# Kernel optimization log

Measured on AMD Instinct MI355X. Metric: run time of the kernel, lower is better.

Reference implementation:

```python
import jax, jax.numpy as jnp
import numpy as np

N = 8388608          # number of samples (2**23)
T_MAX = 100000       # number of distinct time values -> ~84 ties per time


def setup_inputs() -> dict:
    key = jax.random.key(0)
    k1, k2, k3 = jax.random.split(key, 3)
    inp = jax.random.normal(k1, (N,), dtype=jnp.float32)            # log hazards
    target = jax.random.randint(k2, (N,), 0, T_MAX, dtype=jnp.int32)  # times
    weight = jax.random.randint(k3, (N,), 0, 2, dtype=jnp.int32)      # event indicator
    return {"input": inp, "target": target, "weight": weight}


def _cox_efron_npll(log_hz, time, event):
    """Negative Cox partial log-likelihood with Efron tie correction, mean reduction.

    Faithful to torchsurv's _partial_likelihood_efron: per unique time j,
    pll_j = sum_{i in H_j} log_hz_i - sum_{l=0}^{m_j-1} log(D_j - (l/m_j)*T_j)
    where H_j = events at time j, D_j = sum of exp(log_hz) over risk set (t>=t_j),
    T_j = sum of exp(log_hz) over H_j, m_j = |H_j|; loss = -mean over j with m_j>0.
    """
    n = log_hz.shape[0]
    order = jnp.argsort(time)                       # sort by time (group-sum math is tie-order invariant)
    t = time[order]
    lh = log_hz[order]
    ev = event[order].astype(lh.dtype)

    # group id per sample: 0..(num_unique-1), padded groups beyond that are empty
    new_grp = jnp.concatenate([jnp.zeros((1,), jnp.int32), (t[1:] != t[:-1]).astype(jnp.int32)])
    seg = jnp.cumsum(new_grp)                       # [n] int32

    hz = jnp.exp(lh)
    grp_hz = jax.ops.segment_sum(hz, seg, num_segments=n)          # sum exp per time group
    denom_naive = jnp.cumsum(grp_hz[::-1])[::-1]                   # risk-set sums (suffix over groups)
    m = jax.ops.segment_sum(ev, seg, num_segments=n)               # events per group
    log_nom = jax.ops.segment_sum(lh * ev, seg, num_segments=n)    # sum of log_hz over H_j
    ties = jax.ops.segment_sum(hz * ev, seg, num_segments=n)       # sum of exp over H_j

    # rank l in [0, m_j) of each event within its group
    csum_e = jnp.cumsum(ev)
    events_before = jnp.concatenate([jnp.zeros((1,), lh.dtype), jnp.cumsum(m)[:-1]])
    rank = csum_e - 1.0 - events_before[seg]
    mg = jnp.maximum(m[seg], 1.0)
    term = jnp.where(ev > 0.0,
                     jnp.log(denom_naive[seg] - (rank / mg) * ties[seg]),
                     0.0)
    log_denom = jax.ops.segment_sum(term, seg, num_segments=n)

    include = (m > 0.0).astype(lh.dtype)
    pll = jnp.where(m > 0.0, log_nom - log_denom, 0.0)
    # reduction='mean': -pll.nanmean() over groups that contain events
    return -(jnp.sum(pll) / jnp.sum(include))


def reference(input, target, weight):
    return _cox_efron_npll(input, target, weight)
```

## Files before the change

kernel.cpp:

```cpp
#include <hip/hip_runtime.h>

#define TMAXV 100000
#define CHUNK 256
#define NCHUNK ((TMAXV + CHUNK - 1) / CHUNK)
#define WB 256
#define LOGWB 8
#define SB ((TMAXV + WB - 1) / WB)
#define SBP 512
#define TILE 4096
#define RPT 16
#define KS 8
#define CAP 4096
#define RPH (CAP / 256)


__device__ __forceinline__ float block_reduce_sum(float v, float* sdata) {
    int lane = threadIdx.x & 63;
    int wid  = threadIdx.x >> 6;
    #pragma unroll
    for (int off = 32; off > 0; off >>= 1)
        v += __shfl_down(v, off, 64);
    if (lane == 0) sdata[wid] = v;
    __syncthreads();
    if (wid == 0) {
        v = (lane < 4) ? sdata[lane] : 0.0f;
        v += __shfl_down(v, 2, 64);
        v += __shfl_down(v, 1, 64);
    }
    return v;
}

__device__ __forceinline__ double block_reduce_sum_d(double v, double* sdata) {
    int lane = threadIdx.x & 63;
    int wid  = threadIdx.x >> 6;
    #pragma unroll
    for (int off = 32; off > 0; off >>= 1)
        v += __shfl_down(v, off, 64);
    if (lane == 0) sdata[wid] = v;
    __syncthreads();
    if (wid == 0) {
        v = (lane < 4) ? sdata[lane] : 0.0;
        v += __shfl_down(v, 2, 64);
        v += __shfl_down(v, 1, 64);
    }
    return v;
}

__device__ __forceinline__ unsigned encode_rec(float x, int t, int e) {
    float h = __expf(x);
    return (__float_as_uint(h) & 0x7FFFFF00u)
         | (unsigned)(t & (WB - 1))
         | ((unsigned)e << 31);
}


__global__ void count_pfx_kernel(const int* __restrict__ tgt,
                                 int* __restrict__ pfx_arr,
                                 int* __restrict__ cnt_t, int n) {
    __shared__ int lc[SBP];
    __shared__ int ls[SBP];
    int tid = threadIdx.x, tile = blockIdx.x;
    lc[tid] = 0; lc[tid + 256] = 0;
    __syncthreads();
    int lo = tile * TILE;
    if (lo + TILE <= n) {
        const int4* tgt4 = (const int4*)(tgt + lo);
        #pragma unroll
        for (int q = 0; q < RPT / 4; ++q) {
            int4 t4 = tgt4[q * 256 + tid];
            atomicAdd(&lc[t4.x >> LOGWB], 1);
            atomicAdd(&lc[t4.y >> LOGWB], 1);
            atomicAdd(&lc[t4.z >> LOGWB], 1);
            atomicAdd(&lc[t4.w >> LOGWB], 1);
        }
    } else {
        int hi = min(n, lo + TILE);
        for (int i = lo + tid; i < hi; i += 256)
            atomicAdd(&lc[tgt[i] >> LOGWB], 1);
    }
    __syncthreads();
    int c0 = lc[tid], c1 = lc[tid + 256];
    int i1 = tid + 256;
    ls[tid] = c0; ls[i1] = c1;
    __syncthreads();
    for (int off = 1; off < SBP; off <<= 1) {
        int a0 = (tid >= off) ? ls[tid - off] : 0;
        int a1 = (i1  >= off) ? ls[i1  - off] : 0;
        __syncthreads();
        ls[tid] += a0; ls[i1] += a1;
        __syncthreads();
    }
    size_t rb = (size_t)tile * SBP;
    pfx_arr[rb + tid] = ls[tid] - c0;
    pfx_arr[rb + i1]  = ls[i1]  - c1;
    cnt_t[rb + tid] = c0;
    cnt_t[rb + i1]  = c1;
}

__global__ void tile_scan_direct_kernel(const int* __restrict__ cnt_t,
                                        int* __restrict__ tilebase_s,
                                        int* __restrict__ totals, int nt) {
    __shared__ int ls[256];
    int s = blockIdx.x, tid = threadIdx.x;
    int run = 0;
    for (int t0 = 0; t0 < nt; t0 += 256) {
        int t = t0 + tid;
        int c = (t < nt) ? cnt_t[(size_t)t * SBP + s] : 0;
        ls[tid] = c;
        __syncthreads();
        for (int off = 1; off < 256; off <<= 1) {
            int a = (tid >= off) ? ls[tid - off] : 0;
            __syncthreads();
            ls[tid] += a;
            __syncthreads();
        }
        int incl = ls[tid];
        int tot  = ls[255];
        if (t < nt) tilebase_s[(size_t)s * nt + t] = run + incl - c;
        run += tot;
        __syncthreads();
    }
    if (tid == 0) totals[s] = run;
}

__global__ void bucket_base_kernel(const int* __restrict__ totals,
                                   int* __restrict__ base, int n) {
    __shared__ int ls[SBP];
    int tid = threadIdx.x;
    int c = totals[tid];
    ls[tid] = c;
    __syncthreads();
    for (int off = 1; off < SBP; off <<= 1) {
        int a = (tid >= off) ? ls[tid - off] : 0;
        __syncthreads();
        ls[tid] += a;
        __syncthreads();
    }
    base[tid] = ls[tid] - c;
    if (tid == 0) base[SBP] = n;
}

__global__ void scatter_kernel(const float* __restrict__ lh,
                               const int*   __restrict__ tgt,
                               const int*   __restrict__ ev,
                               const int*   __restrict__ pfx_arr,
                               const int*   __restrict__ tilebase_s,
                               const int*   __restrict__ base,
                               unsigned* __restrict__ val,
                               double* __restrict__ acc, int n, int nt) {
    __shared__ unsigned fu[TILE];
    __shared__ unsigned short bidv[TILE];
    __shared__ int pfx[SBP];
    __shared__ int tb[SBP];
    __shared__ int lrank[SBP];
    __shared__ float sdata[4];
    int tid  = threadIdx.x;
    int tile = blockIdx.x;
    int lo   = tile * TILE;
    int cnt_here = min(TILE, n - lo);
    int i1 = tid + 256;
    size_t rb = (size_t)tile * SBP;

    pfx[tid] = pfx_arr[rb + tid];
    pfx[i1]  = pfx_arr[rb + i1];
    tb[tid]  = base[tid] + tilebase_s[(size_t)tid * nt + tile];
    tb[i1]   = base[i1]  + tilebase_s[(size_t)i1  * nt + tile];
    lrank[tid] = 0; lrank[i1] = 0;

    unsigned rbits[RPT];
    int      rk[RPT];
    float xl = 0.f;
    if (lo + TILE <= n) {
        const int4*   tgt4 = (const int4*)(tgt + lo);
        const int4*   ev4  = (const int4*)(ev + lo);
        const float4* lh4  = (const float4*)(lh + lo);
        #pragma unroll
        for (int q = 0; q < RPT / 4; ++q) {
            int idx = q * 256 + tid;
            int4   t4 = tgt4[idx];
            int4   e4 = ev4[idx];
            float4 x4 = lh4[idx];
            rbits[q*4+0] = encode_rec(x4.x, t4.x, e4.x & 1); rk[q*4+0] = t4.x >> LOGWB; if (e4.x & 1) xl += x4.x;
            rbits[q*4+1] = encode_rec(x4.y, t4.y, e4.y & 1); rk[q*4+1] = t4.y >> LOGWB; if (e4.y & 1) xl += x4.y;
            rbits[q*4+2] = encode_rec(x4.z, t4.z, e4.z & 1); rk[q*4+2] = t4.z >> LOGWB; if (e4.z & 1) xl += x4.z;
            rbits[q*4+3] = encode_rec(x4.w, t4.w, e4.w & 1); rk[q*4+3] = t4.w >> LOGWB; if (e4.w & 1) xl += x4.w;
        }
    } else {
        #pragma unroll
        for (int k = 0; k < RPT; ++k) {
            int i = lo + k * 256 + tid;
            if (i < n) {
                int t = tgt[i]; int e = ev[i] & 1; float x = lh[i];
                rbits[k] = encode_rec(x, t, e);
                rk[k] = t >> LOGWB;
                if (e) xl += x;
            } else rk[k] = -1;
        }
    }
    __syncthreads();

    #pragma unroll
    for (int k = 0; k < RPT; ++k) {
        if (rk[k] >= 0) {
            int b = rk[k];
            int r = atomicAdd(&lrank[b], 1);
            int pos = pfx[b] + r;
            fu[pos]   = rbits[k];
            bidv[pos] = (unsigned short)b;
        }
    }
    __syncthreads();

    int pairs = cnt_here >> 1;
    const uint2* fu2 = (const uint2*)fu;
    const unsigned* bid2 = (const unsigned*)bidv;
    for (int q = tid; q < pairs; q += 256) {
        uint2 bb = fu2[q];
        unsigned bp = bid2[q];
        int b0 = (int)(bp & 0xFFFFu);
        int b1 = (int)(bp >> 16);
        int p0 = q * 2;
        val[tb[b0] + (p0     - pfx[b0])] = bb.x;
        val[tb[b1] + (p0 + 1 - pfx[b1])] = bb.y;
    }
    if ((cnt_here & 1) && tid == 0) {
        int p = cnt_here - 1;
        int b = (int)bidv[p];
        val[tb[b] + (p - pfx[b])] = fu[p];
    }

    float rl = block_reduce_sum(xl, sdata);
    if (tid == 0) atomicAdd(&acc[2], (double)rl);
}

__global__ void bucket_hist_kernel(const unsigned* __restrict__ val,
                                   const int* __restrict__ base,
                                   float* __restrict__ partials,
                                   float* __restrict__ chunk_sum) {
    __shared__ unsigned fv[CAP];
    __shared__ unsigned cnt[WB];
    __shared__ unsigned rankc[WB];
    __shared__ unsigned pfx[WB];
    __shared__ unsigned ls[WB];
    __shared__ float sdata[4];
    int tid = threadIdx.x;
    int b   = blockIdx.x >> 3;
    int k   = blockIdx.x & (KS - 1);
    int lo0 = base[b], len = base[b + 1] - lo0;
    int lo  = lo0 + (int)(((long long)len * k) / KS);
    int hi  = lo0 + (int)(((long long)len * (k + 1)) / KS);

    float sh = 0.f, cm = 0.f, th = 0.f;

    for (int c0 = lo; c0 < hi; c0 += CAP) {
        int c1 = min(hi, c0 + CAP);
        cnt[tid] = 0; rankc[tid] = 0;
        __syncthreads();

        unsigned rv[RPH];
        int      rs[RPH];
        #pragma unroll
        for (int u = 0; u < RPH; ++u) {
            int i = c0 + u * 256 + tid;
            if (i < c1) {
                rv[u] = val[i];
                rs[u] = (int)(rv[u] & (WB - 1));
                atomicAdd(&cnt[rs[u]], 1u);
            } else {
                rs[u] = -1;
            }
        }
        __syncthreads();

        unsigned c = cnt[tid];
        ls[tid] = c;
        __syncthreads();
        for (int off = 1; off < 256; off <<= 1) {
            unsigned a = (tid >= off) ? ls[tid - off] : 0u;
            __syncthreads();
            ls[tid] += a;
            __syncthreads();
        }
        pfx[tid] = ls[tid] - c;
        __syncthreads();

        #pragma unroll
        for (int u = 0; u < RPH; ++u) {
            if (rs[u] >= 0) {
                unsigned r = atomicAdd(&rankc[rs[u]], 1u);
                fv[pfx[rs[u]] + r] = rv[u];
            }
        }
        __syncthreads();

        int s0 = (int)pfx[tid], e0 = s0 + (int)cnt[tid];
        for (int p = s0; p < e0; ++p) {
            unsigned bits = fv[p];
            float h = fabsf(__uint_as_float(bits));
            sh += h;
            if (bits >> 31) { cm += 1.0f; th += h; }
        }
        __syncthreads();
    }

    float* pbase = partials + (size_t)blockIdx.x * 3 * WB;
    pbase[0 * WB + tid] = sh;
    pbase[1 * WB + tid] = cm;
    pbase[2 * WB + tid] = th;

    float st = block_reduce_sum(sh, sdata);
    if (tid == 0) unsafeAtomicAdd(&chunk_sum[b], st);
}

__global__ void pll_suffix_kernel(const float* __restrict__ partials,
                                  const float* __restrict__ chunk_sum,
                                  double* __restrict__ acc) {
    __shared__ float sf[CHUNK];
    __shared__ float sdata[4];
    __shared__ float sdata2[4];
    __shared__ double dsd[4];
    __shared__ double doff;
    int tid = threadIdx.x;
    int b   = blockIdx.x;
    float sh = 0.f, cm = 0.f, th = 0.f;
    #pragma unroll
    for (int k = 0; k < KS; ++k) {
        const float* pbase = partials + (size_t)(b * KS + k) * 3 * WB;
        sh += pbase[0 * WB + tid];
        cm += pbase[1 * WB + tid];
        th += pbase[2 * WB + tid];
    }
    sf[tid] = sh;
    __syncthreads();
    for (int off = 1; off < CHUNK; off <<= 1) {
        float add = (tid + off < CHUNK) ? sf[tid + off] : 0.0f;
        __syncthreads();
        sf[tid] += add;
        __syncthreads();
    }
    double mysum = 0.0;
    for (int j = b + 1 + tid; j < NCHUNK; j += 256)
        mysum += (double)chunk_sum[j];
    double red = block_reduce_sum_d(mysum, dsd);
    if (tid == 0) doff = red;
    __syncthreads();
    double off_d = doff;

    int t = b * CHUNK + tid;
    float pll = 0.0f, inc = 0.0f;
    if (t < TMAXV && cm > 0.5f) {
        float D    = (float)(off_d + (double)sf[tid]);
        int   mi   = (int)(cm + 0.5f);
        float step = th / cm;
        float s = 0.0f;
        for (int l = 0; l < mi; ++l)
            s += __logf(D - (float)l * step);
        pll = -s;
        inc = 1.0f;
    }
    float rp = block_reduce_sum(pll, sdata);
    __syncthreads();
    float ri = block_reduce_sum(inc, sdata2);
    if (threadIdx.x == 0) {
        atomicAdd(&acc[0], (double)rp);
        atomicAdd(&acc[1], (double)ri);
    }
}

__global__ void finalize_kernel(const double* __restrict__ acc,
                                float* __restrict__ out) {
    double cnt = acc[1];
    out[0] = (cnt > 0.0) ? (float)(-(acc[0] + acc[2]) / cnt) : 0.0f;
}

__global__ void hist_kernel(const float* __restrict__ lh,
                            const int*   __restrict__ tgt,
                            const int*   __restrict__ ev,
                            float* __restrict__ sum_hz,
                            float* __restrict__ mcnt,
                            float* __restrict__ log_nom,
                            float* __restrict__ ties,
                            int n) {
    int i = blockIdx.x * blockDim.x + threadIdx.x;
    if (i >= n) return;
    float x = lh[i];
    int   t = tgt[i];
    int   e = ev[i];
    float h = __expf(x);
    unsafeAtomicAdd(&sum_hz[t], h);
    if (e) {
        unsafeAtomicAdd(&mcnt[t], 1.0f);
        unsafeAtomicAdd(&log_nom[t], x);
        unsafeAtomicAdd(&ties[t], h);
    }
}

__global__ void chunk_sum_kernel(const float* __restrict__ sum_hz,
                                 float* __restrict__ chunk_sum) {
    __shared__ float sdata[4];
    int i = blockIdx.x * CHUNK + threadIdx.x;
    float v = (i < TMAXV) ? sum_hz[i] : 0.0f;
    v = block_reduce_sum(v, sdata);
    if (threadIdx.x == 0) chunk_sum[blockIdx.x] = v;
}

__global__ void chunk_scan_kernel(const float* __restrict__ chunk_sum,
                                  double* __restrict__ chunk_off) {
    __shared__ double ds[512];
    int tid = threadIdx.x;
    double own = (tid < NCHUNK) ? (double)chunk_sum[tid] : 0.0;
    ds[tid] = own;
    __syncthreads();
    for (int off = 1; off < 512; off <<= 1) {
        double add = (tid + off < 512) ? ds[tid + off] : 0.0;
        __syncthreads();
        ds[tid] += add;
        __syncthreads();
    }
    if (tid < NCHUNK) chunk_off[tid] = ds[tid] - own;
}

__global__ void pll_kernel(const float* __restrict__ mcnt,
                           const float* __restrict__ log_nom,
                           const float* __restrict__ ties,
                           const float* __restrict__ sum_hz,
                           const double* __restrict__ chunk_off,
                           double* __restrict__ acc) {
    __shared__ float sf[CHUNK];
    __shared__ float sdata[4];
    __shared__ float sdata2[4];
    int tid = threadIdx.x;
    int t   = blockIdx.x * CHUNK + tid;
    float v = (t < TMAXV) ? sum_hz[t] : 0.0f;
    sf[tid] = v;
    __syncthreads();
    for (int off = 1; off < CHUNK; off <<= 1) {
        float add = (tid + off < CHUNK) ? sf[tid + off] : 0.0f;
        __syncthreads();
        sf[tid] += add;
        __syncthreads();
    }
    float pll = 0.0f, inc = 0.0f;
    if (t < TMAXV) {
        float mv = mcnt[t];
        if (mv > 0.5f) {
            float D    = (float)(chunk_off[blockIdx.x] + (double)sf[tid]);
            float T    = ties[t];
            int   mi   = (int)(mv + 0.5f);
            float step = T / mv;
            float s = 0.0f;
            for (int l = 0; l < mi; ++l)
                s += __logf(D - (float)l * step);
            pll = log_nom[t] - s;
            inc = 1.0f;
        }
    }
    float rp = block_reduce_sum(pll, sdata);
    __syncthreads();
    float ri = block_reduce_sum(inc, sdata2);
    if (threadIdx.x == 0) {
        atomicAdd(&acc[0], (double)rp);
        atomicAdd(&acc[1], (double)ri);
    }
}

extern "C" void kernel_launch(void* const* d_in, const int* in_sizes, int n_in,
                              void* d_out, int out_size, void* d_ws, size_t ws_size,
                              hipStream_t stream) {
    const float* lh  = (const float*)d_in[0];
    const int*   tgt = (const int*)d_in[1];
    const int*   ev  = (const int*)d_in[2];
    float*       out = (float*)d_out;
    int n  = in_sizes[0];
    int nt = (n + TILE - 1) / TILE;

    char* ws = (char*)d_ws;
    size_t off = 0;
    auto take = [&](size_t bytes, size_t align) {
        off = (off + align - 1) & ~(align - 1);
        size_t r = off; off += bytes; return r;
    };
    size_t o_acc    = take(32, 16);
    size_t o_csum   = take((size_t)SBP * 4, 16);
    size_t zero_bytes = off;
    size_t o_base   = take((size_t)(SBP + 1) * 4, 16);
    size_t o_totals = take((size_t)SBP * 4, 16);
    size_t o_pfx    = take((size_t)nt * SBP * 4, 16);
    size_t o_cntt   = take((size_t)nt * SBP * 4, 16);
    size_t o_tbs    = take((size_t)nt * SBP * 4, 16);
    size_t o_val    = take((size_t)n * 4, 16);
    size_t need     = off;
    size_t part_sz  = (size_t)SB * KS * 3 * WB * 4;
    size_t o_part   = o_pfx;
    if (o_part + part_sz > need) need = o_part + part_sz;

    if (ws_size >= need) {
        double*   acc       = (double*)(ws + o_acc);
        float*    chunk_sum = (float*)(ws + o_csum);
        int*      base      = (int*)(ws + o_base);
        int*      totals    = (int*)(ws + o_totals);
        int*      pfx_arr   = (int*)(ws + o_pfx);
        int*      cnt_t     = (int*)(ws + o_cntt);
        int*      tilebase_s= (int*)(ws + o_tbs);
        unsigned* val       = (unsigned*)(ws + o_val);
        float*    partials  = (float*)(ws + o_part);

        hipMemsetAsync(d_ws, 0, zero_bytes, stream);

        count_pfx_kernel<<<nt, 256, 0, stream>>>(tgt, pfx_arr, cnt_t, n);
        tile_scan_direct_kernel<<<SBP, 256, 0, stream>>>(cnt_t, tilebase_s, totals, nt);
        bucket_base_kernel<<<1, SBP, 0, stream>>>(totals, base, n);
        scatter_kernel<<<nt, 256, 0, stream>>>(lh, tgt, ev, pfx_arr, tilebase_s, base,
                                               val, acc, n, nt);
        bucket_hist_kernel<<<SB * KS, 256, 0, stream>>>(val, base, partials, chunk_sum);
        pll_suffix_kernel<<<NCHUNK, 256, 0, stream>>>(partials, chunk_sum, acc);
        finalize_kernel<<<1, 1, 0, stream>>>(acc, out);
    } else {
        size_t f = 0;
        auto ftake = [&](size_t bytes, size_t align) {
            f = (f + align - 1) & ~(align - 1);
            size_t r = f; f += bytes; return r;
        };
        size_t f_acc  = ftake(32, 16);
        size_t f_sum  = ftake((size_t)TMAXV * 4, 16);
        size_t f_m    = ftake((size_t)TMAXV * 4, 16);
        size_t f_ln   = ftake((size_t)TMAXV * 4, 16);
        size_t f_ties = ftake((size_t)TMAXV * 4, 16);
        size_t zb     = f;
        size_t f_csum = ftake((size_t)NCHUNK * 4, 16);
        size_t f_coff = ftake((size_t)NCHUNK * 8, 8);

        double* acc     = (double*)(ws + f_acc);
        float*  sum_hz  = (float*)(ws + f_sum);
        float*  mcnt    = (float*)(ws + f_m);
        float*  log_nom = (float*)(ws + f_ln);
        float*  ties    = (float*)(ws + f_ties);
        float*  chunk_sum = (float*)(ws + f_csum);
        double* chunk_off = (double*)(ws + f_coff);

        hipMemsetAsync(d_ws, 0, zb, stream);

        hist_kernel<<<(n + 255) / 256, 256, 0, stream>>>(lh, tgt, ev, sum_hz, mcnt, log_nom, ties, n);
        chunk_sum_kernel<<<NCHUNK, 256, 0, stream>>>(sum_hz, chunk_sum);
        chunk_scan_kernel<<<1, 512, 0, stream>>>(chunk_sum, chunk_off);
        pll_kernel<<<NCHUNK, 256, 0, stream>>>(mcnt, log_nom, ties, sum_hz, chunk_off, acc);
        finalize_kernel<<<1, 1, 0, stream>>>(acc, out);
    }
}
```

Baseline: 214.6 us.

## Widen radix buckets, fuse scans and finalize, replace local sort with LDS atomics

Buckets are widened from 256 to 512 time values, so there are 256 superbuckets per tile, one per thread. The workspace memset moves into the count kernel. The bucket-base scan joins the tile scan through a last-block-done counter, and finalize joins the suffix kernel the same way, which removes three launches. The scatter path writes to LDS straight after load and keeps 8-bit bucket ids. The per-bucket local counting sort in the histogram kernel becomes shared-memory float atomics that feed global atomic accumulators, so the partials buffer is gone. The risks are LDS atomic contention, float atomics making summation order nondeterministic, and the zeroing now depending on the count kernel's grid-stride loop running before later kernels.

After: 300.5 us. 1.4x slower.

```diff
diff --git a/kernel.cpp b/kernel.cpp
--- a/kernel.cpp
+++ b/kernel.cpp
@@ -3,15 +3,13 @@
 #define TMAXV 100000
 #define CHUNK 256
 #define NCHUNK ((TMAXV + CHUNK - 1) / CHUNK)
-#define WB 256
-#define LOGWB 8
+#define WB 512
+#define LOGWB 9
 #define SB ((TMAXV + WB - 1) / WB)
-#define SBP 512
+#define SBP 256
 #define TILE 4096
 #define RPT 16
 #define KS 8
-#define CAP 4096
-#define RPH (CAP / 256)
 
 
 __device__ __forceinline__ float block_reduce_sum(float v, float* sdata) {
@@ -48,7 +46,7 @@
 
 __device__ __forceinline__ unsigned encode_rec(float x, int t, int e) {
     float h = __expf(x);
-    return (__float_as_uint(h) & 0x7FFFFF00u)
+    return (__float_as_uint(h) & 0x7FFFFE00u)
          | (unsigned)(t & (WB - 1))
          | ((unsigned)e << 31);
 }
@@ -56,11 +54,15 @@
 
 __global__ void count_pfx_kernel(const int* __restrict__ tgt,
                                  int* __restrict__ pfx_arr,
-                                 int* __restrict__ cnt_t, int n) {
+                                 int* __restrict__ cnt_t,
+                                 unsigned* __restrict__ zero_base,
+                                 int nzero_dw, int n) {
     __shared__ int lc[SBP];
     __shared__ int ls[SBP];
     int tid = threadIdx.x, tile = blockIdx.x;
-    lc[tid] = 0; lc[tid + 256] = 0;
+    for (int i = tile * 256 + tid; i < nzero_dw; i += gridDim.x * 256)
+        zero_base[i] = 0u;
+    lc[tid] = 0;
     __syncthreads();
     int lo = tile * TILE;
     if (lo + TILE <= n) {
@@ -79,33 +81,62 @@
             atomicAdd(&lc[tgt[i] >> LOGWB], 1);
     }
     __syncthreads();
-    int c0 = lc[tid], c1 = lc[tid + 256];
-    int i1 = tid + 256;
-    ls[tid] = c0; ls[i1] = c1;
+    int c0 = lc[tid];
+    ls[tid] = c0;
     __syncthreads();
     for (int off = 1; off < SBP; off <<= 1) {
-        int a0 = (tid >= off) ? ls[tid - off] : 0;
-        int a1 = (i1  >= off) ? ls[i1  - off] : 0;
-        __syncthreads();
-        ls[tid] += a0; ls[i1] += a1;
+        int a = (tid >= off) ? ls[tid - off] : 0;
+        __syncthreads();
+        ls[tid] += a;
         __syncthreads();
     }
     size_t rb = (size_t)tile * SBP;
     pfx_arr[rb + tid] = ls[tid] - c0;
-    pfx_arr[rb + i1]  = ls[i1]  - c1;
     cnt_t[rb + tid] = c0;
-    cnt_t[rb + i1]  = c1;
-}
-
-__global__ void tile_scan_direct_kernel(const int* __restrict__ cnt_t,
-                                        int* __restrict__ tilebase_s,
-                                        int* __restrict__ totals, int nt) {
+}
+
+__global__ void tile_scan_kernel(const int* __restrict__ cnt_t,
+                                 int* __restrict__ tilebase_t,
+                                 int* __restrict__ totals,
+                                 int* __restrict__ base,
+                                 unsigned* __restrict__ done,
+                                 int nt, int n) {
     __shared__ int ls[256];
+    __shared__ int lastFlag;
     int s = blockIdx.x, tid = threadIdx.x;
     int run = 0;
-    for (int t0 = 0; t0 < nt; t0 += 256) {
-        int t = t0 + tid;
-        int c = (t < nt) ? cnt_t[(size_t)t * SBP + s] : 0;
+    for (int t0 = 0; t0 < nt; t0 += 8 * 256) {
+        int cv[8];
+        #pragma unroll
+        for (int u = 0; u < 8; ++u) {
+            int t = t0 + u * 256 + tid;
+            cv[u] = (t < nt) ? cnt_t[(size_t)t * SBP + s] : 0;
+        }
+        #pragma unroll
+        for (int u = 0; u < 8; ++u) {
+            int t = t0 + u * 256 + tid;
+            int c = cv[u];
+            ls[tid] = c;
+            __syncthreads();
+            for (int off = 1; off < 256; off <<= 1) {
+                int a = (tid >= off) ? ls[tid - off] : 0;
+                __syncthreads();
+                ls[tid] += a;
+                __syncthreads();
+            }
+            if (t < nt) tilebase_t[(size_t)t * SBP + s] = run + ls[tid] - c;
+            run += ls[255];
+            __syncthreads();
+        }
+    }
+    if (tid == 0) {
+        __hip_atomic_store(&totals[s], run, __ATOMIC_RELEASE, __HIP_MEMORY_SCOPE_AGENT);
+        unsigned prev = __hip_atomic_fetch_add(done, 1u, __ATOMIC_ACQ_REL, __HIP_MEMORY_SCOPE_AGENT);
+        lastFlag = (prev == (unsigned)(gridDim.x - 1)) ? 1 : 0;
+    }
+    __syncthreads();
+    if (lastFlag) {
+        int c = __hip_atomic_load(&totals[tid], __ATOMIC_ACQUIRE, __HIP_MEMORY_SCOPE_AGENT);
         ls[tid] = c;
         __syncthreads();
         for (int off = 1; off < 256; off <<= 1) {
@@ -114,42 +145,21 @@
             ls[tid] += a;
             __syncthreads();
         }
-        int incl = ls[tid];
-        int tot  = ls[255];
-        if (t < nt) tilebase_s[(size_t)s * nt + t] = run + incl - c;
-        run += tot;
-        __syncthreads();
-    }
-    if (tid == 0) totals[s] = run;
-}
-
-__global__ void bucket_base_kernel(const int* __restrict__ totals,
-                                   int* __restrict__ base, int n) {
-    __shared__ int ls[SBP];
-    int tid = threadIdx.x;
-    int c = totals[tid];
-    ls[tid] = c;
-    __syncthreads();
-    for (int off = 1; off < SBP; off <<= 1) {
-        int a = (tid >= off) ? ls[tid - off] : 0;
-        __syncthreads();
-        ls[tid] += a;
-        __syncthreads();
-    }
-    base[tid] = ls[tid] - c;
-    if (tid == 0) base[SBP] = n;
+        base[tid] = ls[tid] - c;
+        if (tid == 0) base[SBP] = n;
+    }
 }
 
 __global__ void scatter_kernel(const float* __restrict__ lh,
                                const int*   __restrict__ tgt,
                                const int*   __restrict__ ev,
                                const int*   __restrict__ pfx_arr,
-                               const int*   __restrict__ tilebase_s,
+                               const int*   __restrict__ tilebase_t,
                                const int*   __restrict__ base,
                                unsigned* __restrict__ val,
                                double* __restrict__ acc, int n, int nt) {
     __shared__ unsigned fu[TILE];
-    __shared__ unsigned short bidv[TILE];
+    __shared__ unsigned char bidv[TILE];
     __shared__ int pfx[SBP];
     __shared__ int tb[SBP];
     __shared__ int lrank[SBP];
@@ -158,17 +168,13 @@
     int tile = blockIdx.x;
     int lo   = tile * TILE;
     int cnt_here = min(TILE, n - lo);
-    int i1 = tid + 256;
     size_t rb = (size_t)tile * SBP;
 
-    pfx[tid] = pfx_arr[rb + tid];
-    pfx[i1]  = pfx_arr[rb + i1];
-    tb[tid]  = base[tid] + tilebase_s[(size_t)tid * nt + tile];
-    tb[i1]   = base[i1]  + tilebase_s[(size_t)i1  * nt + tile];
-    lrank[tid] = 0; lrank[i1] = 0;
-
-    unsigned rbits[RPT];
-    int      rk[RPT];
+    pfx[tid]   = pfx_arr[rb + tid];
+    tb[tid]    = base[tid] + tilebase_t[rb + tid];
+    lrank[tid] = 0;
+    __syncthreads();
+
     float xl = 0.f;
     if (lo + TILE <= n) {
         const int4*   tgt4 = (const int4*)(tgt + lo);
@@ -180,10 +186,26 @@
             int4   t4 = tgt4[idx];
             int4   e4 = ev4[idx];
             float4 x4 = lh4[idx];
-            rbits[q*4+0] = encode_rec(x4.x, t4.x, e4.x & 1); rk[q*4+0] = t4.x >> LOGWB; if (e4.x & 1) xl += x4.x;
-            rbits[q*4+1] = encode_rec(x4.y, t4.y, e4.y & 1); rk[q*4+1] = t4.y >> LOGWB; if (e4.y & 1) xl += x4.y;
-            rbits[q*4+2] = encode_rec(x4.z, t4.z, e4.z & 1); rk[q*4+2] = t4.z >> LOGWB; if (e4.z & 1) xl += x4.z;
-            rbits[q*4+3] = encode_rec(x4.w, t4.w, e4.w & 1); rk[q*4+3] = t4.w >> LOGWB; if (e4.w & 1) xl += x4.w;
+            {
+                int b = t4.x >> LOGWB; unsigned r = encode_rec(x4.x, t4.x, e4.x & 1);
+                int k = atomicAdd(&lrank[b], 1); int pos = pfx[b] + k;
+                fu[pos] = r; bidv[pos] = (unsigned char)b; if (e4.x & 1) xl += x4.x;
+            }
+            {
+                int b = t4.y >> LOGWB; unsigned r = encode_rec(x4.y, t4.y, e4.y & 1);
+                int k = atomicAdd(&lrank[b], 1); int pos = pfx[b] + k;
+                fu[pos] = r; bidv[pos] = (unsigned char)b; if (e4.y & 1) xl += x4.y;
+            }
+            {
+                int b = t4.z >> LOGWB; unsigned r = encode_rec(x4.z, t4.z, e4.z & 1);
+                int k = atomicAdd(&lrank[b], 1); int pos = pfx[b] + k;
+                fu[pos] = r; bidv[pos] = (unsigned char)b; if (e4.z & 1) xl += x4.z;
+            }
+            {
+                int b = t4.w >> LOGWB; unsigned r = encode_rec(x4.w, t4.w, e4.w & 1);
+                int k = atomicAdd(&lrank[b], 1); int pos = pfx[b] + k;
+                fu[pos] = r; bidv[pos] = (unsigned char)b; if (e4.w & 1) xl += x4.w;
+            }
         }
     } else {
         #pragma unroll
@@ -191,35 +213,21 @@
             int i = lo + k * 256 + tid;
             if (i < n) {
                 int t = tgt[i]; int e = ev[i] & 1; float x = lh[i];
-                rbits[k] = encode_rec(x, t, e);
-                rk[k] = t >> LOGWB;
-                if (e) xl += x;
-            } else rk[k] = -1;
-        }
-    }
-    __syncthreads();
-
-    #pragma unroll
-    for (int k = 0; k < RPT; ++k) {
-        if (rk[k] >= 0) {
-            int b = rk[k];
-            int r = atomicAdd(&lrank[b], 1);
-            int pos = pfx[b] + r;
-            fu[pos]   = rbits[k];
-            bidv[pos] = (unsigned short)b;
+                int b = t >> LOGWB; unsigned r = encode_rec(x, t, e);
+                int rr = atomicAdd(&lrank[b], 1); int pos = pfx[b] + rr;
+                fu[pos] = r; bidv[pos] = (unsigned char)b; if (e) xl += x;
+            }
         }
     }
     __syncthreads();
 
     int pairs = cnt_here >> 1;
     const uint2* fu2 = (const uint2*)fu;
-    const unsigned* bid2 = (const unsigned*)bidv;
     for (int q = tid; q < pairs; q += 256) {
         uint2 bb = fu2[q];
-        unsigned bp = bid2[q];
-        int b0 = (int)(bp & 0xFFFFu);
-        int b1 = (int)(bp >> 16);
         int p0 = q * 2;
+        int b0 = (int)bidv[p0];
+        int b1 = (int)bidv[p0 + 1];
         val[tb[b0] + (p0     - pfx[b0])] = bb.x;
         val[tb[b1] + (p0 + 1 - pfx[b1])] = bb.y;
     }
@@ -235,14 +243,15 @@
 
 __global__ void bucket_hist_kernel(const unsigned* __restrict__ val,
                                    const int* __restrict__ base,
-                                   float* __restrict__ partials,
+                                   float* __restrict__ sh_g,
+                                   float* __restrict__ cm_g,
+                                   float* __restrict__ th_g,
                                    float* __restrict__ chunk_sum) {
-    __shared__ unsigned fv[CAP];
-    __shared__ unsigned cnt[WB];
-    __shared__ unsigned rankc[WB];
-    __shared__ unsigned pfx[WB];
-    __shared__ unsigned ls[WB];
+    __shared__ float sh[WB];
+    __shared__ float cm[WB];
+    __shared__ float th[WB];
     __shared__ float sdata[4];
+    __shared__ float sdata2[4];
     int tid = threadIdx.x;
     int b   = blockIdx.x >> 3;
     int k   = blockIdx.x & (KS - 1);
@@ -250,71 +259,47 @@
     int lo  = lo0 + (int)(((long long)len * k) / KS);
     int hi  = lo0 + (int)(((long long)len * (k + 1)) / KS);
 
-    float sh = 0.f, cm = 0.f, th = 0.f;
-
-    for (int c0 = lo; c0 < hi; c0 += CAP) {
-        int c1 = min(hi, c0 + CAP);
-        cnt[tid] = 0; rankc[tid] = 0;
-        __syncthreads();
-
-        unsigned rv[RPH];
-        int      rs[RPH];
-        #pragma unroll
-        for (int u = 0; u < RPH; ++u) {
-            int i = c0 + u * 256 + tid;
-            if (i < c1) {
-                rv[u] = val[i];
-                rs[u] = (int)(rv[u] & (WB - 1));
-                atomicAdd(&cnt[rs[u]], 1u);
-            } else {
-                rs[u] = -1;
-            }
-        }
-        __syncthreads();
-
-        unsigned c = cnt[tid];
-        ls[tid] = c;
-        __syncthreads();
-        for (int off = 1; off < 256; off <<= 1) {
-            unsigned a = (tid >= off) ? ls[tid - off] : 0u;
-            __syncthreads();
-            ls[tid] += a;
-            __syncthreads();
-        }
-        pfx[tid] = ls[tid] - c;
-        __syncthreads();
-
-        #pragma unroll
-        for (int u = 0; u < RPH; ++u) {
-            if (rs[u] >= 0) {
-                unsigned r = atomicAdd(&rankc[rs[u]], 1u);
-                fv[pfx[rs[u]] + r] = rv[u];
-            }
-        }
-        __syncthreads();
-
-        int s0 = (int)pfx[tid], e0 = s0 + (int)cnt[tid];
-        for (int p = s0; p < e0; ++p) {
-            unsigned bits = fv[p];
-            float h = fabsf(__uint_as_float(bits));
-            sh += h;
-            if (bits >> 31) { cm += 1.0f; th += h; }
-        }
-        __syncthreads();
-    }
-
-    float* pbase = partials + (size_t)blockIdx.x * 3 * WB;
-    pbase[0 * WB + tid] = sh;
-    pbase[1 * WB + tid] = cm;
-    pbase[2 * WB + tid] = th;
-
-    float st = block_reduce_sum(sh, sdata);
-    if (tid == 0) unsafeAtomicAdd(&chunk_sum[b], st);
-}
-
-__global__ void pll_suffix_kernel(const float* __restrict__ partials,
+    sh[tid] = 0.f; sh[tid + 256] = 0.f;
+    cm[tid] = 0.f; cm[tid + 256] = 0.f;
+    th[tid] = 0.f; th[tid + 256] = 0.f;
+    __syncthreads();
+
+    for (int i = lo + tid; i < hi; i += 256) {
+        unsigned bits = val[i];
+        int   s = (int)(bits & (WB - 1));
+        float h = fabsf(__uint_as_float(bits));
+        atomicAdd(&sh[s], h);
+        if (bits >> 31) {
+            atomicAdd(&cm[s], 1.0f);
+            atomicAdd(&th[s], h);
+        }
+    }
+    __syncthreads();
+
+    int t0 = b * WB + tid;
+    unsafeAtomicAdd(&sh_g[t0],       sh[tid]);
+    unsafeAtomicAdd(&sh_g[t0 + 256], sh[tid + 256]);
+    unsafeAtomicAdd(&cm_g[t0],       cm[tid]);
+    unsafeAtomicAdd(&cm_g[t0 + 256], cm[tid + 256]);
+    unsafeAtomicAdd(&th_g[t0],       th[tid]);
+    unsafeAtomicAdd(&th_g[t0 + 256], th[tid + 256]);
+
+    float r0 = block_reduce_sum(sh[tid], sdata);
+    __syncthreads();
+    float r1 = block_reduce_sum(sh[tid + 256], sdata2);
+    if (tid == 0) {
+        unsafeAtomicAdd(&chunk_sum[2 * b],     r0);
+        unsafeAtomicAdd(&chunk_sum[2 * b + 1], r1);
+    }
+}
+
+__global__ void pll_suffix_kernel(const float* __restrict__ sh_g,
+                                  const float* __restrict__ cm_g,
+                                  const float* __restrict__ th_g,
                                   const float* __restrict__ chunk_sum,
-                                  double* __restrict__ acc) {
+                                  double* __restrict__ acc,
+                                  unsigned* __restrict__ done,
+                                  float* __restrict__ out) {
     __shared__ float sf[CHUNK];
     __shared__ float sdata[4];
     __shared__ float sdata2[4];
@@ -322,14 +307,10 @@
     __shared__ double doff;
     int tid = threadIdx.x;
     int b   = blockIdx.x;
-    float sh = 0.f, cm = 0.f, th = 0.f;
-    #pragma unroll
-    for (int k = 0; k < KS; ++k) {
-        const float* pbase = partials + (size_t)(b * KS + k) * 3 * WB;
-        sh += pbase[0 * WB + tid];
-        cm += pbase[1 * WB + tid];
-        th += pbase[2 * WB + tid];
-    }
+    int t   = b * CHUNK + tid;
+    float sh = sh_g[t];
+    float cm = cm_g[t];
+    float th = th_g[t];
     sf[tid] = sh;
     __syncthreads();
     for (int off = 1; off < CHUNK; off <<= 1) {
@@ -346,7 +327,6 @@
     __syncthreads();
     double off_d = doff;
 
-    int t = b * CHUNK + tid;
     float pll = 0.0f, inc = 0.0f;
     if (t < TMAXV && cm > 0.5f) {
         float D    = (float)(off_d + (double)sf[tid]);
@@ -361,9 +341,17 @@
     float rp = block_reduce_sum(pll, sdata);
     __syncthreads();
     float ri = block_reduce_sum(inc, sdata2);
-    if (threadIdx.x == 0) {
+    if (tid == 0) {
         atomicAdd(&acc[0], (double)rp);
         atomicAdd(&acc[1], (double)ri);
+        __threadfence();
+        unsigned prev = __hip_atomic_fetch_add(done, 1u, __ATOMIC_ACQ_REL, __HIP_MEMORY_SCOPE_AGENT);
+        if (prev == (unsigned)(gridDim.x - 1)) {
+            double a0 = __hip_atomic_load(&acc[0], __ATOMIC_ACQUIRE, __HIP_MEMORY_SCOPE_AGENT);
+            double a1 = __hip_atomic_load(&acc[1], __ATOMIC_RELAXED, __HIP_MEMORY_SCOPE_AGENT);
+            double a2 = __hip_atomic_load(&acc[2], __ATOMIC_RELAXED, __HIP_MEMORY_SCOPE_AGENT);
+            out[0] = (a1 > 0.0) ? (float)(-(a0 + a2) / a1) : 0.0f;
+        }
     }
 }
 
@@ -480,8 +468,12 @@
         off = (off + align - 1) & ~(align - 1);
         size_t r = off; off += bytes; return r;
     };
-    size_t o_acc    = take(32, 16);
-    size_t o_csum   = take((size_t)SBP * 4, 16);
+    size_t o_acc   = take(32, 16);
+    size_t o_done  = take(16, 16);
+    size_t o_csum  = take((size_t)512 * 4, 16);
+    size_t o_shg   = take((size_t)SB * WB * 4, 16);
+    size_t o_cmg   = take((size_t)SB * WB * 4, 16);
+    size_t o_thg   = take((size_t)SB * WB * 4, 16);
     size_t zero_bytes = off;
     size_t o_base   = take((size_t)(SBP + 1) * 4, 16);
     size_t o_totals = take((size_t)SBP * 4, 16);
@@ -490,31 +482,31 @@
     size_t o_tbs    = take((size_t)nt * SBP * 4, 16);
     size_t o_val    = take((size_t)n * 4, 16);
     size_t need     = off;
-    size_t part_sz  = (size_t)SB * KS * 3 * WB * 4;
-    size_t o_part   = o_pfx;
-    if (o_part + part_sz > need) need = o_part + part_sz;
 
     if (ws_size >= need) {
         double*   acc       = (double*)(ws + o_acc);
+        unsigned* done      = (unsigned*)(ws + o_done);
         float*    chunk_sum = (float*)(ws + o_csum);
+        float*    sh_g      = (float*)(ws + o_shg);
+        float*    cm_g      = (float*)(ws + o_cmg);
+        float*    th_g      = (float*)(ws + o_thg);
         int*      base      = (int*)(ws + o_base);
         int*      totals    = (int*)(ws + o_totals);
         int*      pfx_arr   = (int*)(ws + o_pfx);
         int*      cnt_t     = (int*)(ws + o_cntt);
-        int*      tilebase_s= (int*)(ws + o_tbs);
+        int*      tilebase_t= (int*)(ws + o_tbs);
         unsigned* val       = (unsigned*)(ws + o_val);
-        float*    partials  = (float*)(ws + o_part);
-
-        hipMemsetAsync(d_ws, 0, zero_bytes, stream);
-
-        count_pfx_kernel<<<nt, 256, 0, stream>>>(tgt, pfx_arr, cnt_t, n);
-        tile_scan_direct_kernel<<<SBP, 256, 0, stream>>>(cnt_t, tilebase_s, totals, nt);
-        bucket_base_kernel<<<1, SBP, 0, stream>>>(totals, base, n);
-        scatter_kernel<<<nt, 256, 0, stream>>>(lh, tgt, ev, pfx_arr, tilebase_s, base,
+
+        count_pfx_kernel<<<nt, 256, 0, stream>>>(tgt, pfx_arr, cnt_t,
+                                                 (unsigned*)ws, (int)(zero_bytes / 4), n);
+        tile_scan_kernel<<<SBP, 256, 0, stream>>>(cnt_t, tilebase_t, totals, base,
+                                                  done + 0, nt, n);
+        scatter_kernel<<<nt, 256, 0, stream>>>(lh, tgt, ev, pfx_arr, tilebase_t, base,
                                                val, acc, n, nt);
-        bucket_hist_kernel<<<SB * KS, 256, 0, stream>>>(val, base, partials, chunk_sum);
-        pll_suffix_kernel<<<NCHUNK, 256, 0, stream>>>(partials, chunk_sum, acc);
-        finalize_kernel<<<1, 1, 0, stream>>>(acc, out);
+        bucket_hist_kernel<<<SB * KS, 256, 0, stream>>>(val, base, sh_g, cm_g, th_g,
+                                                        chunk_sum);
+        pll_suffix_kernel<<<NCHUNK, 256, 0, stream>>>(sh_g, cm_g, th_g, chunk_sum,
+                                                      acc, done + 1, out);
     } else {
         size_t f = 0;
         auto ftake = [&](size_t bytes, size_t align) {
```
